# Optimization experiments

Hardware: AMD Instinct MI355X
Metric: run time of the kernel (lower is better)

Reference implementation:

```python
import jax, jax.numpy as jnp
import numpy as np

B, S, D, O, E, K = 4, 2048, 1024, 1024, 8, 2


def setup_inputs() -> dict:
    key = jax.random.key(0)
    ks = jax.random.split(key, 5)
    scale_in = 1.0 / np.sqrt(D)
    x = jax.random.normal(ks[0], (B, S, D), dtype=jnp.float32)
    gate_w = jax.random.uniform(ks[1], (E, D), jnp.float32, -scale_in, scale_in)
    gate_b = jax.random.uniform(ks[2], (E,), jnp.float32, -scale_in, scale_in)
    expert_w = jax.random.uniform(ks[3], (E, D, O), jnp.float32, -scale_in, scale_in)
    expert_b = jax.random.uniform(ks[4], (E, O), jnp.float32, -scale_in, scale_in)
    return {"x": x, "gate_w": gate_w, "gate_b": gate_b,
            "expert_w": expert_w, "expert_b": expert_b}


def reference(x, gate_w, gate_b, expert_w, expert_b):
    # router logits: [B,S,E]
    logits = jnp.einsum('bsd,ed->bse', x, gate_w) + gate_b
    if K < E:
        topv, topi = jax.lax.top_k(logits, K)           # [B,S,K]
        # scatter top-k logits into -inf; equivalent to keeping only top-k entries
        keep = jax.nn.one_hot(topi, E, dtype=jnp.float32).sum(axis=-2)  # [B,S,E]
        logits = jnp.where(keep > 0, logits, -jnp.inf)
    gate_score = jax.nn.softmax(logits, axis=-1)        # [B,S,E]
    # dense expert computation: [B,S,E,O]
    expert_out = jnp.einsum('bsd,edo->bseo', x, expert_w) + expert_b
    out = jnp.einsum('bseo,bse->bso', expert_out, gate_score)
    return out
```

## Files before the change

kernel.cpp:

```cpp
#include <hip/hip_runtime.h>
#include <stdint.h>

#define T_TOK 8192
#define DD 1024
#define OO 1024
#define EE 8
#define CAP 8192
#define BM 64
#define BN 128
#define BK 64

typedef __attribute__((ext_vector_type(8))) short short8;
typedef __attribute__((ext_vector_type(4))) float f32x4;

__device__ __forceinline__ unsigned short f2b(float f){
  union { float f; unsigned u; } v; v.f = f;
  unsigned r = v.u + 0x7FFFu + ((v.u >> 16) & 1u);
  return (unsigned short)(r >> 16);
}
__device__ __forceinline__ float b2f(unsigned short us){
  union { unsigned u; float f; } v; v.u = ((unsigned)us) << 16; return v.f;
}

__device__ __forceinline__ void gld16(const void* g, void* l){
  __builtin_amdgcn_global_load_lds(
      (const __attribute__((address_space(1))) unsigned int*)g,
      (__attribute__((address_space(3))) unsigned int*)l,
      16, 0, 0);
}

__global__ __launch_bounds__(256) void prep_kernel(
    const float* __restrict__ x, const float* __restrict__ gw, const float* __restrict__ gb,
    const float* __restrict__ ew,
    int2* __restrict__ e01, float2* __restrict__ w01,
    unsigned short* __restrict__ xb, unsigned short* __restrict__ wt)
{
  __shared__ float smem[EE * DD];
  const int tid = threadIdx.x;
  const int b = blockIdx.x;

  if (b < T_TOK / 4) {
    for (int i = tid; i < EE * DD / 4; i += 256)
      ((float4*)smem)[i] = ((const float4*)gw)[i];
    __syncthreads();
    const int wid = tid >> 6, l = tid & 63;
    const int t = b * 4 + wid;
    double acc[EE];
    #pragma unroll
    for (int e = 0; e < EE; ++e) acc[e] = 0.0;
    const float4* xr = (const float4*)(x + (size_t)t * DD);
    ushort4* xw = (ushort4*)(xb + (size_t)t * DD);
    #pragma unroll
    for (int it = 0; it < 4; ++it){
      float4 xv = xr[it * 64 + l];
      ushort4 r;
      r.x = f2b(xv.x); r.y = f2b(xv.y); r.z = f2b(xv.z); r.w = f2b(xv.w);
      xw[it * 64 + l] = r;
      #pragma unroll
      for (int e = 0; e < EE; ++e){
        float4 g = ((const float4*)(smem + e * DD))[it * 64 + l];
        acc[e] += (double)xv.x * g.x + (double)xv.y * g.y
                + (double)xv.z * g.z + (double)xv.w * g.w;
      }
    }
    #pragma unroll
    for (int off = 32; off > 0; off >>= 1){
      #pragma unroll
      for (int e = 0; e < EE; ++e) acc[e] += __shfl_xor(acc[e], off);
    }
    if (l == 0){
      float lg[EE];
      #pragma unroll
      for (int e = 0; e < EE; ++e) lg[e] = (float)acc[e] + gb[e];
      int e0 = 0; float v0 = lg[0];
      for (int e = 1; e < EE; ++e) if (lg[e] > v0){ v0 = lg[e]; e0 = e; }
      int e1 = -1; float v1 = -3.4e38f;
      for (int e = 0; e < EE; ++e) if (e != e0 && lg[e] > v1){ v1 = lg[e]; e1 = e; }
      float ex = expf(v1 - v0);
      float s = 1.0f + ex;
      e01[t] = make_int2(e0, e1);
      w01[t] = make_float2(1.0f / s, ex / s);
    }
  } else {
    float (*t64)[68] = (float(*)[68])smem;
    const int b2 = b - T_TOK / 4;
    const int e = b2 >> 8;
    const int tt = b2 & 255;
    const int dbase = (tt & 15) * 64;
    const int obase = (tt >> 4) * 64;
    const float* src = ew + ((size_t)e << 20);

    const int f4c = tid & 15;
    const int r0  = tid >> 4;
    #pragma unroll
    for (int s = 0; s < 4; ++s){
      int d = r0 + s * 16;
      float4 v = *(const float4*)(src + (size_t)(dbase + d) * OO + obase + f4c * 4);
      *(float4*)&t64[d][f4c * 4] = v;
    }
    __syncthreads();

    const int o  = tid >> 2;
    const int dc = (tid & 3) * 16;
    unsigned short* dst = wt + ((size_t)e << 20) + (size_t)(obase + o) * DD + dbase + dc;
    short8 lo, hi;
    #pragma unroll
    for (int k = 0; k < 8; ++k) lo[k] = (short)f2b(t64[dc + k][o]);
    #pragma unroll
    for (int k = 0; k < 8; ++k) hi[k] = (short)f2b(t64[dc + 8 + k][o]);
    *(short8*)dst = lo;
    *(short8*)(dst + 8) = hi;
  }
}

__global__ __launch_bounds__(256) void compact_kernel(
    const int2* __restrict__ e01,
    int* __restrict__ counts, int* __restrict__ toks)
{
  const int e = blockIdx.x;
  const int tid = threadIdx.x;
  __shared__ int pre[256];
  const int base = tid * (T_TOK / 256);
  int c = 0;
  #pragma unroll 4
  for (int i = 0; i < T_TOK / 256; ++i){
    int2 ee = e01[base + i];
    c += (ee.x == e || ee.y == e) ? 1 : 0;
  }
  pre[tid] = c;
  __syncthreads();
  #pragma unroll
  for (int off = 1; off < 256; off <<= 1){
    int add = (tid >= off) ? pre[tid - off] : 0;
    __syncthreads();
    pre[tid] += add;
    __syncthreads();
  }
  int pos = pre[tid] - c;
  #pragma unroll 4
  for (int i = 0; i < T_TOK / 256; ++i){
    int2 ee = e01[base + i];
    if (ee.x == e || ee.y == e){
      toks[e * CAP + pos] = (base + i) * 2 + (ee.x == e ? 0 : 1);
      ++pos;
    }
  }
  if (tid == 255) counts[e] = pre[255];
}

__global__ __launch_bounds__(256, 4) void moe_gemm(
    const unsigned short* __restrict__ xb,
    const unsigned short* __restrict__ wtr,
    const int* __restrict__ counts,
    const int* __restrict__ toks,
    unsigned short* __restrict__ part)
{
  const int bid = blockIdx.x;
  const int e  = bid & 7;
  const int r  = bid >> 3;
  const int mt = r >> 3;
  const int nt = r & 7;
  const int cnt = counts[e];
  if (mt * BM >= cnt) return;

  __shared__ __align__(16) unsigned short As[BM * BK];
  __shared__ __align__(16) unsigned short Bs[BN * BK];

  const int tid = threadIdx.x;
  const int wid = tid >> 6;
  const int l = tid & 63;
  const int lb = e * CAP;

  const unsigned short* srcA[2];
  const unsigned short* srcB[4];
  #pragma unroll
  for (int i = 0; i < 2; ++i){
    int rr = i * 32 + wid * 8 + (l >> 3);
    int c = (l & 7) ^ (rr & 7);
    int gr = mt * BM + rr; if (gr > cnt - 1) gr = cnt - 1;
    int tok = toks[lb + gr] >> 1;
    srcA[i] = xb + (size_t)tok * DD + c * 8;
  }
  #pragma unroll
  for (int i = 0; i < 4; ++i){
    int rr = i * 32 + wid * 8 + (l >> 3);
    int c = (l & 7) ^ (rr & 7);
    srcB[i] = wtr + ((size_t)e << 20) + (size_t)(nt * BN + rr) * DD + c * 8;
  }

  f32x4 acc[2][4];
  #pragma unroll
  for (int m = 0; m < 2; ++m)
    #pragma unroll
    for (int n = 0; n < 4; ++n) acc[m][n] = (f32x4)0.0f;

  const int wr = wid >> 1, wc = wid & 1;
  const int rA = l & 15, hi = l >> 4, x7 = l & 7;
  const char* AsB = (const char*)As;
  const char* BsB = (const char*)Bs;

  for (int kb = 0; kb < DD / BK; ++kb){
    __syncthreads();
    #pragma unroll
    for (int i = 0; i < 2; ++i)
      gld16(srcA[i] + kb * BK, As + (i * 32 + wid * 8) * BK);
    #pragma unroll
    for (int i = 0; i < 4; ++i)
      gld16(srcB[i] + kb * BK, Bs + (i * 32 + wid * 8) * BK);
    __syncthreads();
    #pragma unroll
    for (int kk = 0; kk < 2; ++kk){
      short8 af[2], bf[4];
      const int ch = ((kk << 2) + hi) ^ x7;
      #pragma unroll
      for (int m = 0; m < 2; ++m){
        int row = wr * 32 + m * 16 + rA;
        af[m] = *(const short8*)(AsB + row * (BK * 2) + ch * 16);
      }
      #pragma unroll
      for (int n = 0; n < 4; ++n){
        int orow = wc * 64 + n * 16 + rA;
        bf[n] = *(const short8*)(BsB + orow * (BK * 2) + ch * 16);
      }
      #pragma unroll
      for (int m = 0; m < 2; ++m)
        #pragma unroll
        for (int n = 0; n < 4; ++n)
          acc[m][n] = __builtin_amdgcn_mfma_f32_16x16x32_bf16(af[m], bf[n], acc[m][n], 0, 0, 0);
    }
  }

  const int col0 = nt * BN + wc * 64;
  #pragma unroll
  for (int m = 0; m < 2; ++m){
    int rbase = mt * BM + wr * 32 + m * 16 + hi * 4;
    #pragma unroll
    for (int j = 0; j < 4; ++j){
      int rr = rbase + j;
      if (rr < cnt){
        unsigned short* prow = part + (size_t)toks[lb + rr] * OO;
        #pragma unroll
        for (int n = 0; n < 4; ++n)
          prow[col0 + n * 16 + rA] = f2b(acc[m][n][j]);
      }
    }
  }
}

__global__ __launch_bounds__(256) void combine_kernel(
    const unsigned short* __restrict__ part,
    const int2* __restrict__ e01, const float2* __restrict__ w01,
    const float* __restrict__ ebias, float* __restrict__ out)
{
  const int tid = threadIdx.x;
  const int wid = tid >> 6, l = tid & 63;
  const int t = blockIdx.x * 4 + wid;
  const int2 ee = e01[t];
  const float2 ww = w01[t];
  const short8* p0 = (const short8*)(part + ((size_t)t * 2) * OO);
  const short8* p1 = (const short8*)(part + ((size_t)t * 2 + 1) * OO);
  const float4* b0 = (const float4*)(ebias + (size_t)ee.x * OO);
  const float4* b1 = (const float4*)(ebias + (size_t)ee.y * OO);
  float4* o = (float4*)(out + (size_t)t * OO);
  #pragma unroll
  for (int i = 0; i < 2; ++i){
    short8 a = p0[i * 64 + l];
    short8 b = p1[i * 64 + l];
    #pragma unroll
    for (int h = 0; h < 2; ++h){
      int cidx = (i * 64 + l) * 2 + h;
      float4 bb0 = b0[cidx], bb1 = b1[cidx];
      float4 r;
      r.x = ww.x * (b2f((unsigned short)a[h*4+0]) + bb0.x) + ww.y * (b2f((unsigned short)b[h*4+0]) + bb1.x);
      r.y = ww.x * (b2f((unsigned short)a[h*4+1]) + bb0.y) + ww.y * (b2f((unsigned short)b[h*4+1]) + bb1.y);
      r.z = ww.x * (b2f((unsigned short)a[h*4+2]) + bb0.z) + ww.y * (b2f((unsigned short)b[h*4+2]) + bb1.z);
      r.w = ww.x * (b2f((unsigned short)a[h*4+3]) + bb0.w) + ww.y * (b2f((unsigned short)b[h*4+3]) + bb1.w);
      o[cidx] = r;
    }
  }
}

extern "C" void kernel_launch(void* const* d_in, const int* in_sizes, int n_in,
                              void* d_out, int out_size, void* d_ws, size_t ws_size,
                              hipStream_t stream) {
  const float* x     = (const float*)d_in[0];
  const float* gw    = (const float*)d_in[1];
  const float* gb    = (const float*)d_in[2];
  const float* ew    = (const float*)d_in[3];
  const float* ebias = (const float*)d_in[4];
  float* out = (float*)d_out;
  char* ws = (char*)d_ws;

  int*    counts = (int*)ws;
  int*    toks   = (int*)(ws + 1024);
  int2*   e01    = (int2*)(ws + 1024 + EE * CAP * 4);
  float2* w01    = (float2*)(ws + 1024 + EE * CAP * 4 + T_TOK * 8);
  unsigned short* part = (unsigned short*)(ws + (1 << 20));
  unsigned short* xb   = (unsigned short*)(ws + (1 << 20) + ((size_t)2 * T_TOK * OO * 2));
  unsigned short* wtr  = xb + (size_t)T_TOK * DD;

  prep_kernel<<<T_TOK / 4 + 2048, 256, 0, stream>>>(x, gw, gb, ew, e01, w01, xb, wtr);
  compact_kernel<<<EE, 256, 0, stream>>>(e01, counts, toks);
  moe_gemm<<<8192, 256, 0, stream>>>(xb, wtr, counts, toks, part);
  combine_kernel<<<T_TOK / 4, 256, 0, stream>>>(part, e01, w01, ebias, out);
}
```

Measured before the change: 104.6 us.

## Route global stores through relaxed atomic stores and pack GEMM epilogue pairs

Replaces the plain global stores in the prep, compact and GEMM kernels with relaxed agent-scope atomic stores. The weight transpose now writes in 64-bit chunks instead of 128-bit vectors. The GEMM epilogue uses a lane shuffle so even lanes write two bf16 outputs as one 32-bit store, halving the scattered 16-bit writes. The atomic stores may change cache behaviour or force narrower stores, and the extra shuffles add some instruction overhead.

```diff
diff --git a/kernel.cpp b/kernel.cpp
--- a/kernel.cpp
+++ b/kernel.cpp
@@ -12,6 +12,13 @@
 
 typedef __attribute__((ext_vector_type(8))) short short8;
 typedef __attribute__((ext_vector_type(4))) float f32x4;
+
+__device__ __forceinline__ void ast64(void* p, unsigned long long v){
+  __hip_atomic_store((unsigned long long*)p, v, __ATOMIC_RELAXED, __HIP_MEMORY_SCOPE_AGENT);
+}
+__device__ __forceinline__ void ast32(void* p, unsigned v){
+  __hip_atomic_store((unsigned*)p, v, __ATOMIC_RELAXED, __HIP_MEMORY_SCOPE_AGENT);
+}
 
 __device__ __forceinline__ unsigned short f2b(float f){
   union { float f; unsigned u; } v; v.f = f;
@@ -49,13 +56,13 @@
     #pragma unroll
     for (int e = 0; e < EE; ++e) acc[e] = 0.0;
     const float4* xr = (const float4*)(x + (size_t)t * DD);
-    ushort4* xw = (ushort4*)(xb + (size_t)t * DD);
+    unsigned short* xw = xb + (size_t)t * DD;
     #pragma unroll
     for (int it = 0; it < 4; ++it){
       float4 xv = xr[it * 64 + l];
-      ushort4 r;
-      r.x = f2b(xv.x); r.y = f2b(xv.y); r.z = f2b(xv.z); r.w = f2b(xv.w);
-      xw[it * 64 + l] = r;
+      union { ushort4 s; unsigned long long u; } r;
+      r.s.x = f2b(xv.x); r.s.y = f2b(xv.y); r.s.z = f2b(xv.z); r.s.w = f2b(xv.w);
+      ast64(xw + (it * 64 + l) * 4, r.u);
       #pragma unroll
       for (int e = 0; e < EE; ++e){
         float4 g = ((const float4*)(smem + e * DD))[it * 64 + l];
@@ -78,8 +85,10 @@
       for (int e = 0; e < EE; ++e) if (e != e0 && lg[e] > v1){ v1 = lg[e]; e1 = e; }
       float ex = expf(v1 - v0);
       float s = 1.0f + ex;
-      e01[t] = make_int2(e0, e1);
-      w01[t] = make_float2(1.0f / s, ex / s);
+      ast64(&e01[t], (unsigned long long)(unsigned)e0 |
+                     ((unsigned long long)(unsigned)e1 << 32));
+      union { float2 f; unsigned long long u; } w; w.f = make_float2(1.0f / s, ex / s);
+      ast64(&w01[t], w.u);
     }
   } else {
     float (*t64)[68] = (float(*)[68])smem;
@@ -103,13 +112,15 @@
     const int o  = tid >> 2;
     const int dc = (tid & 3) * 16;
     unsigned short* dst = wt + ((size_t)e << 20) + (size_t)(obase + o) * DD + dbase + dc;
-    short8 lo, hi;
-    #pragma unroll
-    for (int k = 0; k < 8; ++k) lo[k] = (short)f2b(t64[dc + k][o]);
-    #pragma unroll
-    for (int k = 0; k < 8; ++k) hi[k] = (short)f2b(t64[dc + 8 + k][o]);
-    *(short8*)dst = lo;
-    *(short8*)(dst + 8) = hi;
+    union { ushort4 s; unsigned long long u; } q;
+    #pragma unroll
+    for (int g = 0; g < 4; ++g){
+      q.s.x = f2b(t64[dc + g * 4 + 0][o]);
+      q.s.y = f2b(t64[dc + g * 4 + 1][o]);
+      q.s.z = f2b(t64[dc + g * 4 + 2][o]);
+      q.s.w = f2b(t64[dc + g * 4 + 3][o]);
+      ast64(dst + g * 4, q.u);
+    }
   }
 }
 
@@ -141,11 +152,11 @@
   for (int i = 0; i < T_TOK / 256; ++i){
     int2 ee = e01[base + i];
     if (ee.x == e || ee.y == e){
-      toks[e * CAP + pos] = (base + i) * 2 + (ee.x == e ? 0 : 1);
+      ast32(&toks[e * CAP + pos], (unsigned)((base + i) * 2 + (ee.x == e ? 0 : 1)));
       ++pos;
     }
   }
-  if (tid == 255) counts[e] = pre[255];
+  if (tid == 255) ast32(&counts[e], (unsigned)pre[255]);
 }
 
 __global__ __launch_bounds__(256, 4) void moe_gemm(
@@ -240,8 +251,14 @@
       if (rr < cnt){
         unsigned short* prow = part + (size_t)toks[lb + rr] * OO;
         #pragma unroll
-        for (int n = 0; n < 4; ++n)
-          prow[col0 + n * 16 + rA] = f2b(acc[m][n][j]);
+        for (int n = 0; n < 4; ++n){
+          float v  = acc[m][n][j];
+          float vo = __shfl_xor(v, 1);
+          if ((l & 1) == 0){
+            unsigned pk = (unsigned)f2b(v) | ((unsigned)f2b(vo) << 16);
+            ast32(prow + col0 + n * 16 + rA, pk);
+          }
+        }
       }
     }
   }
```

New measurement: 131.0 us. +25.2%, slower.
